# Kernel optimization log

Measured on AMD Instinct MI355X. Metric: run time of the kernel, lower is better.

Reference implementation:

```python
import jax, jax.numpy as jnp
import numpy as np

D_MODEL = 1024
H = 16
D_K = D_MODEL // H


def setup_inputs() -> dict:
    key = jax.random.key(0)
    ks = jax.random.split(key, 13)
    B, S = 4, 2048
    scale = 1.0 / np.sqrt(D_MODEL)
    inp = {
        "query": jax.random.normal(ks[0], (B, S, D_MODEL), jnp.float32),
        "key": jax.random.normal(ks[1], (B, S, D_MODEL), jnp.float32),
        "value": jax.random.normal(ks[2], (B, S, D_MODEL), jnp.float32),
        "mask": jax.random.randint(ks[3], (B, S, S), 0, 2, jnp.int32),
        "Wq": jax.random.normal(ks[4], (D_MODEL, D_MODEL), jnp.float32) * scale,
        "bq": jnp.zeros((D_MODEL,), jnp.float32),
        "Wk": jax.random.normal(ks[5], (D_MODEL, D_MODEL), jnp.float32) * scale,
        "bk": jnp.zeros((D_MODEL,), jnp.float32),
        "Wv": jax.random.normal(ks[6], (D_MODEL, D_MODEL), jnp.float32) * scale,
        "bv": jnp.zeros((D_MODEL,), jnp.float32),
        "Wo": jax.random.normal(ks[7], (D_MODEL, D_MODEL), jnp.float32) * scale,
        "bo": jnp.zeros((D_MODEL,), jnp.float32),
    }
    return inp


def _split_heads(x):
    # [B, S, D] -> [B, H, S, d_k]
    B, S, _ = x.shape
    return x.reshape(B, S, H, D_K).transpose(0, 2, 1, 3)


def reference(query, key, value, mask, Wq, bq, Wk, bk, Wv, bv, Wo, bo):
    B, S, _ = query.shape
    q = _split_heads(query @ Wq + bq)
    k = _split_heads(key @ Wk + bk)
    v = _split_heads(value @ Wv + bv)
    # scores: [B, H, S, S]
    scores = jnp.einsum("bhqd,bhkd->bhqk", q, k) / jnp.sqrt(jnp.float32(D_K))
    scores = jnp.where(mask[:, None, :, :] == 0, jnp.float32(-1e9), scores)
    prob = jax.nn.softmax(scores, axis=-1)
    out = jnp.einsum("bhqk,bhkd->bhqd", prob, v)
    out = out.transpose(0, 2, 1, 3).reshape(B, S, D_MODEL)
    return out @ Wo + bo
```

## Files before the change

kernel.cpp:

```cpp
#include <hip/hip_runtime.h>
#include <hip/hip_bf16.h>


typedef __bf16 bf16;
typedef __bf16 bf16x4 __attribute__((ext_vector_type(4)));
typedef __bf16 bf16x8 __attribute__((ext_vector_type(8)));
typedef float f32x4 __attribute__((ext_vector_type(4)));
typedef float f32x16 __attribute__((ext_vector_type(16)));
typedef unsigned int uint;

__device__ __forceinline__ void gload_lds16(const void* g, void* l) {
  __builtin_amdgcn_global_load_lds(
      (__attribute__((address_space(1))) void*)g,
      (__attribute__((address_space(3))) void*)l, 16, 0, 0);
}

__global__ __launch_bounds__(256) void wt_kernel(const float* __restrict__ Wq,
                                                 const float* __restrict__ Wk,
                                                 const float* __restrict__ Wv,
                                                 const float* __restrict__ Wo,
                                                 bf16* __restrict__ wt) {
  __shared__ float tile[64][65];
  const int z = blockIdx.z;
  const float* W = (z == 0) ? Wq : (z == 1) ? Wk : (z == 2) ? Wv : Wo;
  bf16* out = wt + (size_t)z * 1048576;
  const int k0 = blockIdx.x * 64, n0 = blockIdx.y * 64;
  for (int e = threadIdx.x; e < 4096; e += 256) {
    int r = e >> 6, c = e & 63;
    tile[r][c] = W[(size_t)(k0 + r) * 1024 + n0 + c];
  }
  __syncthreads();
  for (int e = threadIdx.x; e < 4096; e += 256) {
    int r = e >> 6, c = e & 63;
    out[(size_t)(n0 + r) * 1024 + k0 + c] = (bf16)tile[c][r];
  }
}

__global__ __launch_bounds__(256) void maskpack_kernel(const int* __restrict__ mask,
                                                       unsigned long long* __restrict__ bits) {
  const int lane = threadIdx.x & 63;
  const int wv = threadIdx.x >> 6;
  const int word0 = blockIdx.x * 16 + wv * 4;
#pragma unroll
  for (int m = 0; m < 4; ++m) {
    int v = mask[(size_t)(word0 + m) * 64 + lane];
    unsigned long long b = __ballot(v != 0);
    if (lane == 0) bits[word0 + m] = b;
  }
}

__global__ __launch_bounds__(512) void qkv_gemm_kernel(
    const float* __restrict__ Aq, const float* __restrict__ Ak, const float* __restrict__ Av,
    const bf16* __restrict__ wt, const float* __restrict__ bqp, const float* __restrict__ bkp,
    const float* __restrict__ bvp, char* __restrict__ qbuf, char* __restrict__ kbuf,
    char* __restrict__ vbuf) {
  __shared__ alignas(16) char smem[32768];
  char* As = smem;
  char* Bs = smem + 16384;
  const int t = threadIdx.x;
  const int w = t >> 6, l = t & 63;
  const int hi = l >> 4, lo = l & 15, l7 = l & 7;
  const int wr = w >> 2, wc = w & 3;
  const int row0 = blockIdx.x * 128;
  const int n0 = blockIdx.y * 128;
  const int z = blockIdx.z;
  const float* A = (z == 0) ? Aq : (z == 1) ? Ak : Av;
  const char* Bb = (const char*)(wt + (size_t)z * 1048576);
  const float* bias = (z == 0) ? bqp : (z == 1) ? bkp : bvp;
  char* ob = (z == 0) ? qbuf : (z == 1) ? kbuf : vbuf;

  const f32x4 fz = {0.f, 0.f, 0.f, 0.f};
  f32x4 acc[4][2];
#pragma unroll
  for (int mi = 0; mi < 4; ++mi)
#pragma unroll
    for (int ni = 0; ni < 2; ++ni) acc[mi][ni] = fz;

  for (int kt = 0; kt < 16; ++kt) {
#pragma unroll
    for (int i = 0; i < 4; ++i) {
      int qq = i * 512 + t;
      int r = qq >> 4, q = qq & 15;
      f32x4 f = *(const f32x4*)(A + (size_t)(row0 + r) * 1024 + kt * 64 + q * 4);
      bf16x4 hq = {(bf16)f[0], (bf16)f[1], (bf16)f[2], (bf16)f[3]};
      *(bf16x4*)(As + r * 128 + ((q * 8) ^ ((r & 7) << 4))) = hq;
    }
#pragma unroll
    for (int i = 0; i < 2; ++i) {
      int c = i * 512 + t;
      int r = c >> 3, s = c & 7;
      gload_lds16(Bb + (size_t)(n0 + r) * 2048 + kt * 128 + ((s ^ (r & 7)) * 16),
                  Bs + (i * 512 + w * 64) * 16);
    }
    __syncthreads();
#pragma unroll
    for (int kk = 0; kk < 2; ++kk) {
      bf16x8 af[4], bfr[2];
#pragma unroll
      for (int mi = 0; mi < 4; ++mi)
        af[mi] = *(const bf16x8*)(As + (wr * 64 + mi * 16 + lo) * 128 +
                                  ((kk * 64 + hi * 16) ^ (l7 << 4)));
#pragma unroll
      for (int ni = 0; ni < 2; ++ni)
        bfr[ni] = *(const bf16x8*)(Bs + (wc * 32 + ni * 16 + lo) * 128 +
                                   ((kk * 64 + hi * 16) ^ (l7 << 4)));
#pragma unroll
      for (int mi = 0; mi < 4; ++mi)
#pragma unroll
        for (int ni = 0; ni < 2; ++ni)
          acc[mi][ni] =
              __builtin_amdgcn_mfma_f32_16x16x32_bf16(af[mi], bfr[ni], acc[mi][ni], 0, 0, 0);
    }
    __syncthreads();
  }

  const float scale = (z == 0) ? 0.18033688011112042f : 1.0f;
#pragma unroll
  for (int mi = 0; mi < 4; ++mi)
#pragma unroll
    for (int ni = 0; ni < 2; ++ni) {
      int gcol = n0 + wc * 32 + ni * 16 + lo;
      float bv = bias[gcol];
#pragma unroll
      for (int j = 0; j < 4; ++j) {
        int grow = row0 + wr * 64 + mi * 16 + hi * 4 + j;
        float v = (acc[mi][ni][j] + bv) * scale;
        int b = grow >> 11, si = grow & 2047, hh = gcol >> 6, d = gcol & 63;
        if (z < 2) {
          ((bf16*)ob)[((((size_t)b * 16 + hh) * 2048 + si) << 6) + d] = (bf16)v;
        } else {
          ((bf16*)ob)[((((size_t)b * 16 + hh) * 64 + d) << 11) + si] = (bf16)v;
        }
      }
    }
}

__global__ __launch_bounds__(512) void gemm3_kernel(const char* __restrict__ Aptr,
                                                    const bf16* __restrict__ Bt,
                                                    const float* __restrict__ bias,
                                                    float* __restrict__ Out) {
  __shared__ alignas(16) char smem[32768];
  char* As = smem;
  char* Bs = smem + 16384;
  const int t = threadIdx.x;
  const int w = t >> 6, l = t & 63;
  const int hi = l >> 4, lo = l & 15, l7 = l & 7;
  const int wr = w >> 2, wc = w & 3;
  const int row0 = blockIdx.x * 128;
  const int n0 = blockIdx.y * 128;

  const f32x4 fz = {0.f, 0.f, 0.f, 0.f};
  f32x4 acc[4][2];
#pragma unroll
  for (int mi = 0; mi < 4; ++mi)
#pragma unroll
    for (int ni = 0; ni < 2; ++ni) acc[mi][ni] = fz;

  for (int kt = 0; kt < 16; ++kt) {
#pragma unroll
    for (int i = 0; i < 2; ++i) {
      int c = i * 512 + t;
      int r = c >> 3, s = c & 7;
      gload_lds16(Aptr + (size_t)(row0 + r) * 2048 + kt * 128 + ((s ^ (r & 7)) * 16),
                  As + (i * 512 + w * 64) * 16);
      gload_lds16((const char*)Bt + (size_t)(n0 + r) * 2048 + kt * 128 + ((s ^ (r & 7)) * 16),
                  Bs + (i * 512 + w * 64) * 16);
    }
    __syncthreads();
#pragma unroll
    for (int kk = 0; kk < 2; ++kk) {
      bf16x8 af[4], bfr[2];
#pragma unroll
      for (int mi = 0; mi < 4; ++mi)
        af[mi] = *(const bf16x8*)(As + (wr * 64 + mi * 16 + lo) * 128 +
                                  ((kk * 64 + hi * 16) ^ (l7 << 4)));
#pragma unroll
      for (int ni = 0; ni < 2; ++ni)
        bfr[ni] = *(const bf16x8*)(Bs + (wc * 32 + ni * 16 + lo) * 128 +
                                   ((kk * 64 + hi * 16) ^ (l7 << 4)));
#pragma unroll
      for (int mi = 0; mi < 4; ++mi)
#pragma unroll
        for (int ni = 0; ni < 2; ++ni)
          acc[mi][ni] =
              __builtin_amdgcn_mfma_f32_16x16x32_bf16(af[mi], bfr[ni], acc[mi][ni], 0, 0, 0);
    }
    __syncthreads();
  }

#pragma unroll
  for (int mi = 0; mi < 4; ++mi)
#pragma unroll
    for (int ni = 0; ni < 2; ++ni) {
      int gcol = n0 + wc * 32 + ni * 16 + lo;
      float bv = bias[gcol];
#pragma unroll
      for (int j = 0; j < 4; ++j) {
        int grow = row0 + wr * 64 + mi * 16 + hi * 4 + j;
        Out[(size_t)grow * 1024 + gcol] = acc[mi][ni][j] + bv;
      }
    }
}

__global__ __launch_bounds__(512) void attn_kernel(const char* __restrict__ qb,
                                                   const char* __restrict__ kb,
                                                   const char* __restrict__ vb,
                                                   const unsigned long long* __restrict__ mbits,
                                                   bf16* __restrict__ out) {
  __shared__ alignas(16) char smem[32768];
  const int t = threadIdx.x;
  const int w = t >> 6, l = t & 63;
  const int q31 = l & 31, hi = l >> 5;
  const int bh = blockIdx.x, b = bh >> 4, h = bh & 15;
  const int q0 = blockIdx.y * 256;
  const int qrow = q0 + w * 32 + q31;

  bf16x8 qf[4];
#pragma unroll
  for (int kc = 0; kc < 4; ++kc)
    qf[kc] = *(const bf16x8*)(qb + (size_t)(bh * 2048 + qrow) * 128 + kc * 32 + hi * 16);

  const f32x16 fz16 = {0.f, 0.f, 0.f, 0.f, 0.f, 0.f, 0.f, 0.f,
                       0.f, 0.f, 0.f, 0.f, 0.f, 0.f, 0.f, 0.f};
  f32x16 o[2];
  o[0] = fz16;
  o[1] = fz16;
  float mreg = -3e38f, ls = 0.f;
  const unsigned long long* mrow = mbits + (size_t)(b * 2048 + qrow) * 32;

  for (int kt2 = 0; kt2 < 16; ++kt2) {
#pragma unroll
    for (int i = 0; i < 2; ++i) {
      int c = i * 512 + t;
      int kr = c >> 3, ks = c & 7;
      gload_lds16(kb + (size_t)(bh * 2048 + kt2 * 128 + kr) * 128 + ((ks ^ (kr & 7)) * 16),
                  smem + (i * 512 + w * 64) * 16);
      int vr = c >> 4, vs = c & 15;
      gload_lds16(vb + (size_t)(bh * 64 + vr) * 4096 + kt2 * 256 + ((vs ^ (vr & 7)) * 16),
                  smem + 16384 + (i * 512 + w * 64) * 16);
    }
    unsigned long long mw01[2] = {mrow[kt2 * 2], mrow[kt2 * 2 + 1]};
    __syncthreads();

#pragma unroll
    for (int h2 = 0; h2 < 2; ++h2) {
      const unsigned long long mw = mw01[h2];

#pragma unroll
      for (int n = 0; n < 2; ++n) {
        f32x16 sc = fz16;
        __builtin_amdgcn_s_setprio(1);
#pragma unroll
        for (int kc = 0; kc < 4; ++kc) {
          bf16x8 kf = *(const bf16x8*)(smem + (h2 * 64 + n * 32 + q31) * 128 +
                                       (((kc * 2 + hi) ^ (q31 & 7)) * 16));
          sc = __builtin_amdgcn_mfma_f32_32x32x16_bf16(kf, qf[kc], sc, 0, 0, 0);
        }
        __builtin_amdgcn_s_setprio(0);

        uint m32 = (uint)(mw >> (n * 32 + 4 * hi));
        float tm = -3e38f;
#pragma unroll
        for (int r = 0; r < 16; ++r) {
          const int bi = (r & 3) + 8 * (r >> 2);
          sc[r] = ((m32 >> bi) & 1u) ? sc[r] : -1e9f;
        }
#pragma unroll
        for (int r = 0; r < 16; r += 2) tm = fmaxf(fmaxf(tm, sc[r]), sc[r + 1]);
        tm = fmaxf(tm, __shfl_xor(tm, 32));

        if (!__all(tm - mreg <= 4.f)) {
          float mn = fmaxf(mreg, tm);
          float scal = __builtin_amdgcn_exp2f(mreg - mn);
          ls *= scal;
          o[0] *= scal;
          o[1] *= scal;
          mreg = mn;
        }

        uint wpk[8];
#pragma unroll
        for (int r2 = 0; r2 < 8; ++r2) {
          float p0 = __builtin_amdgcn_exp2f(sc[2 * r2] - mreg);
          float p1 = __builtin_amdgcn_exp2f(sc[2 * r2 + 1] - mreg);
          ls += p0 + p1;
          uint pk;
          asm("v_cvt_pk_bf16_f32 %0, %1, %2" : "=v"(pk) : "v"(p0), "v"(p1));
          wpk[r2] = pk;
        }

        __builtin_amdgcn_s_setprio(1);
#pragma unroll
        for (int c2 = 0; c2 < 2; ++c2) {
          uint a0 = wpk[4 * c2], b0 = wpk[4 * c2 + 2];
          uint a1 = wpk[4 * c2 + 1], b1 = wpk[4 * c2 + 3];
          asm("v_permlane32_swap_b32 %0, %1" : "+v"(a0), "+v"(b0));
          asm("v_permlane32_swap_b32 %0, %1" : "+v"(a1), "+v"(b1));
          union {
            uint u[4];
            bf16x8 v;
          } pf;
          pf.u[0] = a0;
          pf.u[1] = a1;
          pf.u[2] = b0;
          pf.u[3] = b1;
          const int c = n * 2 + c2;
          const int slot = (h2 * 8 + c * 2 + hi);
          bf16x8 vf0 = *(const bf16x8*)(smem + 16384 + q31 * 256 +
                                        ((slot ^ (q31 & 7)) * 16));
          bf16x8 vf1 = *(const bf16x8*)(smem + 16384 + (32 + q31) * 256 +
                                        ((slot ^ (q31 & 7)) * 16));
          o[0] = __builtin_amdgcn_mfma_f32_32x32x16_bf16(vf0, pf.v, o[0], 0, 0, 0);
          o[1] = __builtin_amdgcn_mfma_f32_32x32x16_bf16(vf1, pf.v, o[1], 0, 0, 0);
        }
        __builtin_amdgcn_s_setprio(0);
      }
    }
    __syncthreads();
  }

  ls += __shfl_xor(ls, 32);
  float inv = 1.f / ls;
  size_t rbase = (size_t)((b << 11) + qrow) * 1024 + h * 64;
#pragma unroll
  for (int db = 0; db < 2; ++db)
#pragma unroll
    for (int g = 0; g < 4; ++g) {
      bf16x4 hv = {(bf16)(o[db][4 * g] * inv), (bf16)(o[db][4 * g + 1] * inv),
                   (bf16)(o[db][4 * g + 2] * inv), (bf16)(o[db][4 * g + 3] * inv)};
      *(bf16x4*)(out + rbase + db * 32 + 8 * g + 4 * hi) = hv;
    }
}

extern "C" void kernel_launch(void* const* d_in, const int* in_sizes, int n_in,
                              void* d_out, int out_size, void* d_ws, size_t ws_size,
                              hipStream_t stream) {
  const float* query = (const float*)d_in[0];
  const float* key_ = (const float*)d_in[1];
  const float* value = (const float*)d_in[2];
  const int* mask = (const int*)d_in[3];
  const float* Wq = (const float*)d_in[4];
  const float* bq = (const float*)d_in[5];
  const float* Wk = (const float*)d_in[6];
  const float* bk = (const float*)d_in[7];
  const float* Wv = (const float*)d_in[8];
  const float* bv = (const float*)d_in[9];
  const float* Wo = (const float*)d_in[10];
  const float* bo = (const float*)d_in[11];

  char* ws = (char*)d_ws;
  bf16* wt = (bf16*)ws;
  char* qbuf = ws + 8388608;
  char* kbuf = qbuf + 16777216;
  char* vbuf = kbuf + 16777216;
  char* abuf = vbuf + 16777216;
  unsigned long long* mbits = (unsigned long long*)(abuf + 16777216);

  wt_kernel<<<dim3(16, 16, 4), 256, 0, stream>>>(Wq, Wk, Wv, Wo, wt);
  maskpack_kernel<<<16384, 256, 0, stream>>>(mask, mbits);
  qkv_gemm_kernel<<<dim3(64, 8, 3), 512, 0, stream>>>(query, key_, value, wt, bq, bk, bv,
                                                      qbuf, kbuf, vbuf);
  attn_kernel<<<dim3(64, 8), 512, 0, stream>>>(qbuf, kbuf, vbuf, mbits, (bf16*)abuf);
  gemm3_kernel<<<dim3(64, 8), 512, 0, stream>>>(abuf, wt + 3145728, bo, (float*)d_out);
}
```

Baseline: 269.7 us.

## Pre-cast QKV inputs to bf16 and load A tiles via direct-to-LDS loads

Moves the fp32-to-bf16 conversion of query/key/value out of the projection GEMM into separate cast kernels, so the GEMM can load both A and B tiles with global_load_lds into swizzled shared memory. The single 3-way GEMM launch becomes three sequential cast+GEMM pairs that reuse the attention-output buffer as scratch. This trades extra global traffic (writing and re-reading a bf16 copy of the inputs) and more launches with smaller grids for a simpler, asynchronous A-load path in the GEMM main loop.

```diff
diff --git a/kernel.cpp b/kernel.cpp
--- a/kernel.cpp
+++ b/kernel.cpp
@@ -49,11 +49,20 @@
   }
 }
 
-__global__ __launch_bounds__(512) void qkv_gemm_kernel(
-    const float* __restrict__ Aq, const float* __restrict__ Ak, const float* __restrict__ Av,
-    const bf16* __restrict__ wt, const float* __restrict__ bqp, const float* __restrict__ bkp,
-    const float* __restrict__ bvp, char* __restrict__ qbuf, char* __restrict__ kbuf,
-    char* __restrict__ vbuf) {
+__global__ __launch_bounds__(256) void cast_kernel(const float* __restrict__ in,
+                                                   bf16* __restrict__ out) {
+  const int stride = gridDim.x * 256;
+  for (int i = blockIdx.x * 256 + threadIdx.x; i < 2097152; i += stride) {
+    f32x4 f = *(const f32x4*)(in + (size_t)i * 4);
+    bf16x4 h = {(bf16)f[0], (bf16)f[1], (bf16)f[2], (bf16)f[3]};
+    *(bf16x4*)(out + (size_t)i * 4) = h;
+  }
+}
+
+__global__ __launch_bounds__(512) void qkvg_kernel(const char* __restrict__ Aptr,
+                                                   const bf16* __restrict__ Bt,
+                                                   const float* __restrict__ bias,
+                                                   char* __restrict__ ob, int zmode) {
   __shared__ alignas(16) char smem[32768];
   char* As = smem;
   char* Bs = smem + 16384;
@@ -63,11 +72,6 @@
   const int wr = w >> 2, wc = w & 3;
   const int row0 = blockIdx.x * 128;
   const int n0 = blockIdx.y * 128;
-  const int z = blockIdx.z;
-  const float* A = (z == 0) ? Aq : (z == 1) ? Ak : Av;
-  const char* Bb = (const char*)(wt + (size_t)z * 1048576);
-  const float* bias = (z == 0) ? bqp : (z == 1) ? bkp : bvp;
-  char* ob = (z == 0) ? qbuf : (z == 1) ? kbuf : vbuf;
 
   const f32x4 fz = {0.f, 0.f, 0.f, 0.f};
   f32x4 acc[4][2];
@@ -77,19 +81,13 @@
     for (int ni = 0; ni < 2; ++ni) acc[mi][ni] = fz;
 
   for (int kt = 0; kt < 16; ++kt) {
-#pragma unroll
-    for (int i = 0; i < 4; ++i) {
-      int qq = i * 512 + t;
-      int r = qq >> 4, q = qq & 15;
-      f32x4 f = *(const f32x4*)(A + (size_t)(row0 + r) * 1024 + kt * 64 + q * 4);
-      bf16x4 hq = {(bf16)f[0], (bf16)f[1], (bf16)f[2], (bf16)f[3]};
-      *(bf16x4*)(As + r * 128 + ((q * 8) ^ ((r & 7) << 4))) = hq;
-    }
 #pragma unroll
     for (int i = 0; i < 2; ++i) {
       int c = i * 512 + t;
       int r = c >> 3, s = c & 7;
-      gload_lds16(Bb + (size_t)(n0 + r) * 2048 + kt * 128 + ((s ^ (r & 7)) * 16),
+      gload_lds16(Aptr + (size_t)(row0 + r) * 2048 + kt * 128 + ((s ^ (r & 7)) * 16),
+                  As + (i * 512 + w * 64) * 16);
+      gload_lds16((const char*)Bt + (size_t)(n0 + r) * 2048 + kt * 128 + ((s ^ (r & 7)) * 16),
                   Bs + (i * 512 + w * 64) * 16);
     }
     __syncthreads();
@@ -114,7 +112,7 @@
     __syncthreads();
   }
 
-  const float scale = (z == 0) ? 0.18033688011112042f : 1.0f;
+  const float scale = (zmode == 0) ? 0.18033688011112042f : 1.0f;
 #pragma unroll
   for (int mi = 0; mi < 4; ++mi)
 #pragma unroll
@@ -126,7 +124,7 @@
         int grow = row0 + wr * 64 + mi * 16 + hi * 4 + j;
         float v = (acc[mi][ni][j] + bv) * scale;
         int b = grow >> 11, si = grow & 2047, hh = gcol >> 6, d = gcol & 63;
-        if (z < 2) {
+        if (zmode < 2) {
           ((bf16*)ob)[((((size_t)b * 16 + hh) * 2048 + si) << 6) + d] = (bf16)v;
         } else {
           ((bf16*)ob)[((((size_t)b * 16 + hh) * 64 + d) << 11) + si] = (bf16)v;
@@ -358,8 +356,14 @@
 
   wt_kernel<<<dim3(16, 16, 4), 256, 0, stream>>>(Wq, Wk, Wv, Wo, wt);
   maskpack_kernel<<<16384, 256, 0, stream>>>(mask, mbits);
-  qkv_gemm_kernel<<<dim3(64, 8, 3), 512, 0, stream>>>(query, key_, value, wt, bq, bk, bv,
-                                                      qbuf, kbuf, vbuf);
+
+  cast_kernel<<<2048, 256, 0, stream>>>(query, (bf16*)abuf);
+  qkvg_kernel<<<dim3(64, 8), 512, 0, stream>>>(abuf, wt, bq, qbuf, 0);
+  cast_kernel<<<2048, 256, 0, stream>>>(key_, (bf16*)abuf);
+  qkvg_kernel<<<dim3(64, 8), 512, 0, stream>>>(abuf, wt + 1048576, bk, kbuf, 1);
+  cast_kernel<<<2048, 256, 0, stream>>>(value, (bf16*)abuf);
+  qkvg_kernel<<<dim3(64, 8), 512, 0, stream>>>(abuf, wt + 2097152, bv, vbuf, 2);
+
   attn_kernel<<<dim3(64, 8), 512, 0, stream>>>(qbuf, kbuf, vbuf, mbits, (bf16*)abuf);
   gemm3_kernel<<<dim3(64, 8), 512, 0, stream>>>(abuf, wt + 3145728, bo, (float*)d_out);
 }
```

After: 278.6 us. 3.3% more time.

## Split attention KV tiles across two wave groups in 1024-thread blocks

Applied to the files above, without the earlier changes.

Doubles the attention block to 1024 threads so that two groups of eight waves take alternating KV tiles. Each group keeps its own online-softmax state, and at the end the states are merged through shared memory. Every thread now issues one K and one V load per tile instead of two. The single LDS buffer and the per-tile barriers mean only half the waves compute on any given tile while the rest sit idle. The 1024-thread launch bound also tightens the register budget per wave.

```diff
diff --git a/kernel.cpp b/kernel.cpp
--- a/kernel.cpp
+++ b/kernel.cpp
@@ -202,18 +202,19 @@
     }
 }
 
-__global__ __launch_bounds__(512) void attn_kernel(const char* __restrict__ qb,
-                                                   const char* __restrict__ kb,
-                                                   const char* __restrict__ vb,
-                                                   const unsigned long long* __restrict__ mbits,
-                                                   bf16* __restrict__ out) {
+__global__ __launch_bounds__(1024) void attn_kernel(const char* __restrict__ qb,
+                                                    const char* __restrict__ kb,
+                                                    const char* __restrict__ vb,
+                                                    const unsigned long long* __restrict__ mbits,
+                                                    bf16* __restrict__ out) {
   __shared__ alignas(16) char smem[32768];
   const int t = threadIdx.x;
   const int w = t >> 6, l = t & 63;
+  const int qw = w & 7, pw = w >> 3;
   const int q31 = l & 31, hi = l >> 5;
   const int bh = blockIdx.x, b = bh >> 4, h = bh & 15;
   const int q0 = blockIdx.y * 256;
-  const int qrow = q0 + w * 32 + q31;
+  const int qrow = q0 + qw * 32 + q31;
 
   bf16x8 qf[4];
 #pragma unroll
@@ -228,108 +229,148 @@
   float mreg = -3e38f, ls = 0.f;
   const unsigned long long* mrow = mbits + (size_t)(b * 2048 + qrow) * 32;
 
+  const int kr = t >> 3, ks = t & 7;
+  const int vr = t >> 4, vs = t & 15;
+
   for (int kt2 = 0; kt2 < 16; ++kt2) {
-#pragma unroll
-    for (int i = 0; i < 2; ++i) {
-      int c = i * 512 + t;
-      int kr = c >> 3, ks = c & 7;
-      gload_lds16(kb + (size_t)(bh * 2048 + kt2 * 128 + kr) * 128 + ((ks ^ (kr & 7)) * 16),
-                  smem + (i * 512 + w * 64) * 16);
-      int vr = c >> 4, vs = c & 15;
-      gload_lds16(vb + (size_t)(bh * 64 + vr) * 4096 + kt2 * 256 + ((vs ^ (vr & 7)) * 16),
-                  smem + 16384 + (i * 512 + w * 64) * 16);
-    }
-    unsigned long long mw01[2] = {mrow[kt2 * 2], mrow[kt2 * 2 + 1]};
-    __syncthreads();
-
-#pragma unroll
-    for (int h2 = 0; h2 < 2; ++h2) {
-      const unsigned long long mw = mw01[h2];
-
-#pragma unroll
-      for (int n = 0; n < 2; ++n) {
-        f32x16 sc = fz16;
-        __builtin_amdgcn_s_setprio(1);
-#pragma unroll
-        for (int kc = 0; kc < 4; ++kc) {
-          bf16x8 kf = *(const bf16x8*)(smem + (h2 * 64 + n * 32 + q31) * 128 +
-                                       (((kc * 2 + hi) ^ (q31 & 7)) * 16));
-          sc = __builtin_amdgcn_mfma_f32_32x32x16_bf16(kf, qf[kc], sc, 0, 0, 0);
+    gload_lds16(kb + (size_t)(bh * 2048 + kt2 * 128 + kr) * 128 + ((ks ^ (kr & 7)) * 16),
+                smem + t * 16);
+    gload_lds16(vb + (size_t)(bh * 64 + vr) * 4096 + kt2 * 256 + ((vs ^ (vr & 7)) * 16),
+                smem + 16384 + t * 16);
+    const bool act = (pw == (kt2 & 1));
+    unsigned long long mw01[2] = {0ull, 0ull};
+    if (act) {
+      mw01[0] = mrow[kt2 * 2];
+      mw01[1] = mrow[kt2 * 2 + 1];
+    }
+    __syncthreads();
+
+    if (act) {
+#pragma unroll
+      for (int h2 = 0; h2 < 2; ++h2) {
+        const unsigned long long mw = mw01[h2];
+#pragma unroll
+        for (int n = 0; n < 2; ++n) {
+          f32x16 sc = fz16;
+          __builtin_amdgcn_s_setprio(1);
+#pragma unroll
+          for (int kc = 0; kc < 4; ++kc) {
+            bf16x8 kf = *(const bf16x8*)(smem + (h2 * 64 + n * 32 + q31) * 128 +
+                                         (((kc * 2 + hi) ^ (q31 & 7)) * 16));
+            sc = __builtin_amdgcn_mfma_f32_32x32x16_bf16(kf, qf[kc], sc, 0, 0, 0);
+          }
+          __builtin_amdgcn_s_setprio(0);
+
+          uint m32 = (uint)(mw >> (n * 32 + 4 * hi));
+          float tm = -3e38f;
+#pragma unroll
+          for (int r = 0; r < 16; ++r) {
+            const int bi = (r & 3) + 8 * (r >> 2);
+            sc[r] = ((m32 >> bi) & 1u) ? sc[r] : -1e9f;
+          }
+#pragma unroll
+          for (int r = 0; r < 16; r += 2) tm = fmaxf(fmaxf(tm, sc[r]), sc[r + 1]);
+          tm = fmaxf(tm, __shfl_xor(tm, 32));
+
+          if (!__all(tm - mreg <= 4.f)) {
+            float mn = fmaxf(mreg, tm);
+            float scal = __builtin_amdgcn_exp2f(mreg - mn);
+            ls *= scal;
+            o[0] *= scal;
+            o[1] *= scal;
+            mreg = mn;
+          }
+
+          uint wpk[8];
+#pragma unroll
+          for (int r2 = 0; r2 < 8; ++r2) {
+            float p0 = __builtin_amdgcn_exp2f(sc[2 * r2] - mreg);
+            float p1 = __builtin_amdgcn_exp2f(sc[2 * r2 + 1] - mreg);
+            ls += p0 + p1;
+            uint pk;
+            asm("v_cvt_pk_bf16_f32 %0, %1, %2" : "=v"(pk) : "v"(p0), "v"(p1));
+            wpk[r2] = pk;
+          }
+
+          __builtin_amdgcn_s_setprio(1);
+#pragma unroll
+          for (int c2 = 0; c2 < 2; ++c2) {
+            uint a0 = wpk[4 * c2], b0 = wpk[4 * c2 + 2];
+            uint a1 = wpk[4 * c2 + 1], b1 = wpk[4 * c2 + 3];
+            asm("v_permlane32_swap_b32 %0, %1" : "+v"(a0), "+v"(b0));
+            asm("v_permlane32_swap_b32 %0, %1" : "+v"(a1), "+v"(b1));
+            union {
+              uint u[4];
+              bf16x8 v;
+            } pf;
+            pf.u[0] = a0;
+            pf.u[1] = a1;
+            pf.u[2] = b0;
+            pf.u[3] = b1;
+            const int c = n * 2 + c2;
+            const int slot = (h2 * 8 + c * 2 + hi);
+            bf16x8 vf0 = *(const bf16x8*)(smem + 16384 + q31 * 256 +
+                                          ((slot ^ (q31 & 7)) * 16));
+            bf16x8 vf1 = *(const bf16x8*)(smem + 16384 + (32 + q31) * 256 +
+                                          ((slot ^ (q31 & 7)) * 16));
+            o[0] = __builtin_amdgcn_mfma_f32_32x32x16_bf16(vf0, pf.v, o[0], 0, 0, 0);
+            o[1] = __builtin_amdgcn_mfma_f32_32x32x16_bf16(vf1, pf.v, o[1], 0, 0, 0);
+          }
+          __builtin_amdgcn_s_setprio(0);
         }
-        __builtin_amdgcn_s_setprio(0);
-
-        uint m32 = (uint)(mw >> (n * 32 + 4 * hi));
-        float tm = -3e38f;
-#pragma unroll
-        for (int r = 0; r < 16; ++r) {
-          const int bi = (r & 3) + 8 * (r >> 2);
-          sc[r] = ((m32 >> bi) & 1u) ? sc[r] : -1e9f;
-        }
-#pragma unroll
-        for (int r = 0; r < 16; r += 2) tm = fmaxf(fmaxf(tm, sc[r]), sc[r + 1]);
-        tm = fmaxf(tm, __shfl_xor(tm, 32));
-
-        if (!__all(tm - mreg <= 4.f)) {
-          float mn = fmaxf(mreg, tm);
-          float scal = __builtin_amdgcn_exp2f(mreg - mn);
-          ls *= scal;
-          o[0] *= scal;
-          o[1] *= scal;
-          mreg = mn;
-        }
-
-        uint wpk[8];
-#pragma unroll
-        for (int r2 = 0; r2 < 8; ++r2) {
-          float p0 = __builtin_amdgcn_exp2f(sc[2 * r2] - mreg);
-          float p1 = __builtin_amdgcn_exp2f(sc[2 * r2 + 1] - mreg);
-          ls += p0 + p1;
-          uint pk;
-          asm("v_cvt_pk_bf16_f32 %0, %1, %2" : "=v"(pk) : "v"(p0), "v"(p1));
-          wpk[r2] = pk;
-        }
-
-        __builtin_amdgcn_s_setprio(1);
-#pragma unroll
-        for (int c2 = 0; c2 < 2; ++c2) {
-          uint a0 = wpk[4 * c2], b0 = wpk[4 * c2 + 2];
-          uint a1 = wpk[4 * c2 + 1], b1 = wpk[4 * c2 + 3];
-          asm("v_permlane32_swap_b32 %0, %1" : "+v"(a0), "+v"(b0));
-          asm("v_permlane32_swap_b32 %0, %1" : "+v"(a1), "+v"(b1));
-          union {
-            uint u[4];
-            bf16x8 v;
-          } pf;
-          pf.u[0] = a0;
-          pf.u[1] = a1;
-          pf.u[2] = b0;
-          pf.u[3] = b1;
-          const int c = n * 2 + c2;
-          const int slot = (h2 * 8 + c * 2 + hi);
-          bf16x8 vf0 = *(const bf16x8*)(smem + 16384 + q31 * 256 +
-                                        ((slot ^ (q31 & 7)) * 16));
-          bf16x8 vf1 = *(const bf16x8*)(smem + 16384 + (32 + q31) * 256 +
-                                        ((slot ^ (q31 & 7)) * 16));
-          o[0] = __builtin_amdgcn_mfma_f32_32x32x16_bf16(vf0, pf.v, o[0], 0, 0, 0);
-          o[1] = __builtin_amdgcn_mfma_f32_32x32x16_bf16(vf1, pf.v, o[1], 0, 0, 0);
-        }
-        __builtin_amdgcn_s_setprio(0);
       }
     }
     __syncthreads();
   }
 
   ls += __shfl_xor(ls, 32);
-  float inv = 1.f / ls;
-  size_t rbase = (size_t)((b << 11) + qrow) * 1024 + h * 64;
-#pragma unroll
-  for (int db = 0; db < 2; ++db)
-#pragma unroll
-    for (int g = 0; g < 4; ++g) {
-      bf16x4 hv = {(bf16)(o[db][4 * g] * inv), (bf16)(o[db][4 * g + 1] * inv),
-                   (bf16)(o[db][4 * g + 2] * inv), (bf16)(o[db][4 * g + 3] * inv)};
-      *(bf16x4*)(out + rbase + db * 32 + 8 * g + 4 * hi) = hv;
-    }
+
+  float* xch = (float*)smem;
+  if (pw == 1) {
+    xch[(qw * 64 + l) * 2] = mreg;
+    xch[(qw * 64 + l) * 2 + 1] = ls;
+  }
+  __syncthreads();
+  float s1 = 1.f, s2 = 0.f;
+  if (pw == 0) {
+    float m2 = xch[(qw * 64 + l) * 2];
+    float ls2 = xch[(qw * 64 + l) * 2 + 1];
+    float mm = fmaxf(mreg, m2);
+    s1 = __builtin_amdgcn_exp2f(mreg - mm);
+    s2 = __builtin_amdgcn_exp2f(m2 - mm);
+    ls = ls * s1 + ls2 * s2;
+  }
+  __syncthreads();
+  if (pw == 1) {
+#pragma unroll
+    for (int r = 0; r < 16; ++r) xch[(qw * 64 + l) * 16 + r] = o[0][r];
+  }
+  __syncthreads();
+  if (pw == 0) {
+#pragma unroll
+    for (int r = 0; r < 16; ++r) o[0][r] = o[0][r] * s1 + xch[(qw * 64 + l) * 16 + r] * s2;
+  }
+  __syncthreads();
+  if (pw == 1) {
+#pragma unroll
+    for (int r = 0; r < 16; ++r) xch[(qw * 64 + l) * 16 + r] = o[1][r];
+  }
+  __syncthreads();
+
+  if (pw == 0) {
+#pragma unroll
+    for (int r = 0; r < 16; ++r) o[1][r] = o[1][r] * s1 + xch[(qw * 64 + l) * 16 + r] * s2;
+    float inv = 1.f / ls;
+    size_t rbase = (size_t)((b << 11) + qrow) * 1024 + h * 64;
+#pragma unroll
+    for (int db = 0; db < 2; ++db)
+#pragma unroll
+      for (int g = 0; g < 4; ++g) {
+        bf16x4 hv = {(bf16)(o[db][4 * g] * inv), (bf16)(o[db][4 * g + 1] * inv),
+                     (bf16)(o[db][4 * g + 2] * inv), (bf16)(o[db][4 * g + 3] * inv)};
+        *(bf16x4*)(out + rbase + db * 32 + 8 * g + 4 * hi) = hv;
+      }
+  }
 }
 
 extern "C" void kernel_launch(void* const* d_in, const int* in_sizes, int n_in,
@@ -360,6 +401,6 @@
   maskpack_kernel<<<16384, 256, 0, stream>>>(mask, mbits);
   qkv_gemm_kernel<<<dim3(64, 8, 3), 512, 0, stream>>>(query, key_, value, wt, bq, bk, bv,
                                                       qbuf, kbuf, vbuf);
-  attn_kernel<<<dim3(64, 8), 512, 0, stream>>>(qbuf, kbuf, vbuf, mbits, (bf16*)abuf);
+  attn_kernel<<<dim3(64, 8), 1024, 0, stream>>>(qbuf, kbuf, vbuf, mbits, (bf16*)abuf);
   gemm3_kernel<<<dim3(64, 8), 512, 0, stream>>>(abuf, wt + 3145728, bo, (float*)d_out);
 }
```

Result: slower. 298.9 us (+10.8%).
